# Optimization experiments

Measured on AMD Instinct MI355X. Metric: run time of the kernel, lower is better.

## Reference

```python
import jax, jax.numpy as jnp
import numpy as np

HIDDEN = 3584
NUM_HEADS = 28
NUM_KV_HEADS = 4
HEAD_DIM = 128
ROPE_THETA = 1000000.0
B, S = 2, 2048


def setup_inputs() -> dict:
    key = jax.random.key(0)
    k1, k2, k3, k4 = jax.random.split(key, 4)
    q_size = NUM_HEADS * HEAD_DIM
    kv_size = NUM_KV_HEADS * HEAD_DIM
    return {
        "positions": jnp.arange(B * S, dtype=jnp.int32).reshape(B, S),
        "hidden_states": jax.random.normal(k1, (B, S, HIDDEN), dtype=jnp.float32),
        "w_qkv": jax.random.normal(k2, (HIDDEN, q_size + 2 * kv_size), dtype=jnp.float32) * (HIDDEN ** -0.5),
        "b_qkv": jax.random.normal(k3, (q_size + 2 * kv_size,), dtype=jnp.float32) * 0.02,
        "w_o": jax.random.normal(k4, (q_size, HIDDEN), dtype=jnp.float32) * (q_size ** -0.5),
    }


def _rope_cos_sin(positions):
    # NeoX-style rotary embedding, rotary_dim == head_dim
    half = HEAD_DIM // 2
    inv_freq = 1.0 / (ROPE_THETA ** (jnp.arange(0, half, dtype=jnp.float32) * 2.0 / HEAD_DIM))
    angles = positions.astype(jnp.float32)[..., None] * inv_freq  # [B, S, half]
    return jnp.cos(angles), jnp.sin(angles)


def _apply_rope(x, cos, sin):
    # x: [B, S, H, D]; cos/sin: [B, S, half] -> broadcast over heads
    x1, x2 = jnp.split(x, 2, axis=-1)
    c = cos[:, :, None, :]
    s = sin[:, :, None, :]
    return jnp.concatenate([x1 * c - x2 * s, x2 * c + x1 * s], axis=-1)


def reference(positions, hidden_states, w_qkv, b_qkv, w_o):
    q_size = NUM_HEADS * HEAD_DIM
    kv_size = NUM_KV_HEADS * HEAD_DIM
    scaling = HEAD_DIM ** -0.5
    groups = NUM_HEADS // NUM_KV_HEADS

    qkv = hidden_states @ w_qkv + b_qkv  # [B, S, q+2kv]
    q, k, v = jnp.split(qkv, [q_size, q_size + kv_size], axis=-1)
    q = q.reshape(B, S, NUM_HEADS, HEAD_DIM)
    k = k.reshape(B, S, NUM_KV_HEADS, HEAD_DIM)
    v = v.reshape(B, S, NUM_KV_HEADS, HEAD_DIM)

    cos, sin = _rope_cos_sin(positions)
    q = _apply_rope(q, cos, sin)
    k = _apply_rope(k, cos, sin)

    # GQA: group query heads over kv heads. q: [B, S, Hkv, G, D]
    qg = q.reshape(B, S, NUM_KV_HEADS, groups, HEAD_DIM)
    scores = jnp.einsum("bqhgd,bkhd->bhgqk", qg, k) * scaling  # [B, Hkv, G, S, S]
    causal = jnp.tril(jnp.ones((S, S), dtype=bool))
    scores = jnp.where(causal, scores, jnp.finfo(scores.dtype).min)
    probs = jax.nn.softmax(scores, axis=-1)
    o = jnp.einsum("bhgqk,bkhd->bqhgd", probs, v)  # [B, S, Hkv, G, D]
    o = o.reshape(B, S, NUM_HEADS * HEAD_DIM)
    return o @ w_o  # [B, S, HIDDEN]
```

## Files before the change

kernel.cpp:

```cpp
#include <hip/hip_runtime.h>

typedef unsigned short u16;
typedef unsigned int u32;
typedef __bf16 bf16x8 __attribute__((ext_vector_type(8)));
typedef float f32x4 __attribute__((ext_vector_type(4)));

#define NHEAD 28
#define NKVH 4
#define HD 128
#define NB 2
#define NS 2048
#define NTOK 4096
#define HIDDEN_DIM 3584
#define QKVW 4608
#define QSZ 3584
#define KOFF 3584
#define VOFF 4096
#define VSLAB (NTOK * 512)
#define NJOBS 896
#define ATTN_BLOCKS 768
#define QSCALE_L2E 0.12751744f

__device__ __forceinline__ float bf2f(u16 u) {
  u32 x = ((u32)u) << 16; float f; __builtin_memcpy(&f, &x, 4); return f;
}
__device__ __forceinline__ u16 f2bf(float f) {
  u32 x; __builtin_memcpy(&x, &f, 4);
  x += 0x7FFFu + ((x >> 16) & 1u);
  return (u16)(x >> 16);
}
__device__ __forceinline__ u32 pack2bf(float a, float b) {
  __bf16 lo = (__bf16)a, hi = (__bf16)b;
  u16 ul, uh;
  __builtin_memcpy(&ul, &lo, 2); __builtin_memcpy(&uh, &hi, 2);
  return (u32)ul | ((u32)uh << 16);
}
__device__ __forceinline__ void async16(const void* g, void* lds) {
  __builtin_amdgcn_global_load_lds((const __attribute__((address_space(1))) void*)g,
                                   (__attribute__((address_space(3))) void*)lds,
                                   16, 0, 0);
}

#define SB __builtin_amdgcn_sched_barrier(0)
#define BAR do { SB; __builtin_amdgcn_s_barrier(); SB; } while (0)

__global__ void cast_f32_bf16(const float* __restrict__ in, u16* __restrict__ out) {
  int i = (blockIdx.x * 256 + threadIdx.x) * 4;
  float4 v = *(const float4*)(in + i);
  u32 p0 = (u32)f2bf(v.x) | ((u32)f2bf(v.y) << 16);
  u32 p1 = (u32)f2bf(v.z) | ((u32)f2bf(v.w) << 16);
  uint2 r; r.x = p0; r.y = p1;
  *(uint2*)(out + i) = r;
}

__global__ void transpose_cast(const float* __restrict__ in, u16* __restrict__ out,
                               int R, int C) {
  __shared__ float tile[32][33];
  int tx = threadIdx.x & 31, ty = threadIdx.x >> 5;
  int c0 = blockIdx.x * 32, r0 = blockIdx.y * 32;
#pragma unroll
  for (int i = 0; i < 32; i += 8)
    tile[ty + i][tx] = in[(size_t)(r0 + ty + i) * C + c0 + tx];
  __syncthreads();
#pragma unroll
  for (int i = 0; i < 32; i += 8)
    out[(size_t)(c0 + ty + i) * R + r0 + tx] = f2bf(tile[tx][ty + i]);
}

__global__ void rope_table(const int* __restrict__ positions,
                           float* __restrict__ cs, float* __restrict__ sn,
                           int* __restrict__ ctr) {
  if (blockIdx.x == 0 && threadIdx.x == 0) *ctr = 0;
  int idx = blockIdx.x * 256 + threadIdx.x;
  int t = idx >> 6, i = idx & 63;
  float p = (float)positions[t];
  float inv = expf(-(float)i * (13.815510557964274f / 64.f));
  float a = p * inv;
  cs[idx] = cosf(a);
  sn[idx] = sinf(a);
}

__global__ void rope_kernel(u16* __restrict__ qkv, const float* __restrict__ cs,
                            const float* __restrict__ sn) {
  int w = threadIdx.x >> 6, l = threadIdx.x & 63;
  int rid = blockIdx.x * 4 + w;
  int t = rid >> 5, hh = rid & 31;
  size_t base = (size_t)t * QKVW + (hh < NHEAD ? hh * HD : KOFF + (hh - NHEAD) * HD);
  float x1 = bf2f(qkv[base + l]), x2 = bf2f(qkv[base + l + 64]);
  float c = cs[t * 64 + l], s = sn[t * 64 + l];
  float y1 = x1 * c - x2 * s;
  float y2 = x2 * c + x1 * s;
  if (hh < NHEAD) { y1 *= QSCALE_L2E; y2 *= QSCALE_L2E; }
  qkv[base + l] = f2bf(y1);
  qkv[base + l + 64] = f2bf(y2);
}

template <int MODE>
__global__ __launch_bounds__(512, 2) void gemm256(
    const u16* __restrict__ A, const u16* __restrict__ Bt,
    const float* __restrict__ bias, u16* __restrict__ outb,
    float* __restrict__ outf, int M, int Next, int Kst, int ldc, int NT) {
  __shared__ __align__(16) u16 Al[2][256 * 64];
  __shared__ __align__(16) u16 Bl[2][256 * 64];
  const int tid = threadIdx.x;
  const int l = tid & 63, w = tid >> 6;
  const int g = l >> 4, r = l & 15;
  const int wm = w >> 2, wn = w & 3;
  const int nbx = Next >> 8;
  const int cpx = (int)gridDim.x >> 3;
  const int bid = ((int)blockIdx.x & 7) * cpx + ((int)blockIdx.x >> 3);
  int bx, by, kbase;
  float* outp = outf;
  if (MODE == 2) {
    const int tps = nbx * (M >> 8);
    const int ks = bid / tps, rem = bid % tps;
    by = rem / nbx; bx = rem % nbx;
    kbase = ks * (NT << 6);
    outp = outf + (size_t)ks * M * Next;
  } else {
    bx = bid % nbx; by = bid / nbx; kbase = 0;
  }
  const int row0 = by * 256, col0 = bx * 256;

  f32x4 acc[8][4] = {};
  bf16x8 af[4][2];
  bf16x8 bfr[2][2][2];

  auto stageU = [&](const u16* mb, int base0, char* ldsMat, int h, int t) {
#pragma unroll
    for (int q = 0; q < 2; ++q) {
      const int idx = q * 512 + tid;
      const int rho = h * 128 + (idx >> 3);
      const int sl = (idx & 7) ^ (rho & 7);
      async16(mb + (size_t)(base0 + rho) * Kst + kbase + t * 64 + sl * 8,
              ldsMat + (size_t)(t & 1) * 32768 + h * 16384 + idx * 16);
    }
  };

#define READ_A(s, rh)                                                           \
  _Pragma("unroll") for (int fr = 0; fr < 4; ++fr) {                            \
    const int row_ = (rh) * 128 + wm * 64 + fr * 16 + r;                        \
    _Pragma("unroll") for (int kk = 0; kk < 2; ++kk) {                          \
      const int sl_ = (kk * 4 + g) ^ (row_ & 7);                                \
      af[fr][kk] = *(const bf16x8*)((const char*)Al + (s) * 32768 +             \
                                    row_ * 128 + sl_ * 16);                     \
    }                                                                           \
  }
#define READ_B(s, ch)                                                           \
  _Pragma("unroll") for (int fc = 0; fc < 2; ++fc) {                            \
    const int col_ = (ch) * 128 + wn * 32 + fc * 16 + r;                        \
    _Pragma("unroll") for (int kk = 0; kk < 2; ++kk) {                          \
      const int sl_ = (kk * 4 + g) ^ (col_ & 7);                                \
      bfr[ch][fc][kk] = *(const bf16x8*)((const char*)Bl + (s) * 32768 +        \
                                         col_ * 128 + sl_ * 16);                \
    }                                                                           \
  }
#define MFMA_Q(rh, ch)                                                          \
  __builtin_amdgcn_s_setprio(1);                                                \
  _Pragma("unroll") for (int fr = 0; fr < 4; ++fr)                              \
  _Pragma("unroll") for (int fc = 0; fc < 2; ++fc)                              \
  _Pragma("unroll") for (int kk = 0; kk < 2; ++kk)                              \
    acc[(rh) * 4 + fr][(ch) * 2 + fc] = __builtin_amdgcn_mfma_f32_16x16x32_bf16( \
        af[fr][kk], bfr[ch][fc][kk], acc[(rh) * 4 + fr][(ch) * 2 + fc], 0, 0, 0);\
  __builtin_amdgcn_s_setprio(0);

  stageU(A, row0, (char*)Al, 0, 0); stageU(A, row0, (char*)Al, 1, 0);
  stageU(Bt, col0, (char*)Bl, 0, 0); stageU(Bt, col0, (char*)Bl, 1, 0);
  stageU(A, row0, (char*)Al, 0, 1); stageU(Bt, col0, (char*)Bl, 0, 1);
  SB; asm volatile("s_waitcnt vmcnt(4)" ::: "memory");
  BAR;

  for (int t = 0; t < NT; ++t) {
    const int s = t & 1;
    READ_A(s, 0); READ_B(s, 0);
    if (t + 1 < NT) stageU(A, row0, (char*)Al, 1, t + 1);
    BAR; MFMA_Q(0, 0); BAR;
    READ_B(s, 1);
    if (t + 1 < NT) stageU(Bt, col0, (char*)Bl, 1, t + 1);
    BAR; MFMA_Q(0, 1); BAR;
    READ_A(s, 1);
    if (t + 2 < NT) stageU(A, row0, (char*)Al, 0, t + 2);
    BAR; MFMA_Q(1, 0); BAR;
    if (t + 2 < NT) stageU(Bt, col0, (char*)Bl, 0, t + 2);
    BAR; MFMA_Q(1, 1);
    if (t < NT - 2)        { SB; asm volatile("s_waitcnt vmcnt(4)" ::: "memory"); }
    else if (t == NT - 2)  { SB; asm volatile("s_waitcnt vmcnt(0)" ::: "memory"); }
    BAR;
  }
  SB; asm volatile("s_waitcnt vmcnt(0)" ::: "memory");

#pragma unroll
  for (int m = 0; m < 8; ++m) {
    const int row = row0 + (m >> 2) * 128 + wm * 64 + (m & 3) * 16 + g * 4;
#pragma unroll
    for (int n = 0; n < 4; ++n) {
      const int col = col0 + (n >> 1) * 128 + wn * 32 + (n & 1) * 16 + r;
      const float bb = (MODE == 0) ? bias[col] : 0.f;
#pragma unroll
      for (int j = 0; j < 4; ++j) {
        float v = acc[m][n][j] + bb;
        if (MODE == 0) outb[(size_t)(row + j) * ldc + col] = f2bf(v);
        else           outp[(size_t)(row + j) * ldc + col] = v;
      }
    }
  }
}

__global__ void v_reduce(const float* __restrict__ slabs, const float* __restrict__ bias,
                         u16* __restrict__ vtg) {
  __shared__ float tile[32][33];
  const int tx = threadIdx.x & 31, ty = threadIdx.x >> 5;
  const int c0 = blockIdx.x * 32;
  const int r0 = blockIdx.y * 32;
#pragma unroll
  for (int i = 0; i < 32; i += 8) {
    const size_t idx = (size_t)(r0 + ty + i) * 512 + c0 + tx;
    float s = slabs[idx] + slabs[idx + VSLAB] + slabs[idx + 2 * VSLAB] +
              slabs[idx + 3 * VSLAB];
    tile[ty + i][tx] = s + bias[VOFF + c0 + tx];
  }
  __syncthreads();
#pragma unroll
  for (int i = 0; i < 32; i += 8) {
    const int col = c0 + ty + i;
    const int row = r0 + tx;
    vtg[((size_t)((((row >> 11) * NKVH) + (col >> 7)) * HD + (col & 127))) * NS +
        (row & 2047)] = f2bf(tile[tx][ty + i]);
  }
}

__global__ __launch_bounds__(512) void attn_kernel(const u16* __restrict__ qkv,
                                                   const u16* __restrict__ vtg,
                                                   u16* __restrict__ Oh,
                                                   int* __restrict__ ctr) {
  __shared__ __align__(16) u16 Ks[2][64 * 128];
  __shared__ __align__(16) u16 Vt[128 * 64];
  __shared__ int s_job;
  const int tid = threadIdx.x, l = tid & 63, w = tid >> 6;
  const int g = l >> 4, r = l & 15;
  const int srcA = r + ((l & 16) << 1);
  const int srcB = srcA + 16;
  const bool hi = (l & 32) != 0;

  for (;;) {
    if (tid == 0) s_job = atomicAdd(ctr, 1);
    __syncthreads();
    const int jid = s_job;
    if (jid >= NJOBS) return;
    const int qtr = jid / 56;
    const int qt = 15 - qtr;
    const int bh = jid - qtr * 56;
    const int h = bh % NHEAD, b = bh / NHEAD;
    const int kvh = h / 7;
    const int q0 = qt * 128;

    const int qrow = q0 + w * 16 + r;
    const size_t qbase = (size_t)(b * NS + qrow) * QKVW + h * HD;
    bf16x8 qf[4];
#pragma unroll
    for (int ks = 0; ks < 4; ++ks)
      qf[ks] = *(const bf16x8*)(qkv + qbase + ks * 32 + g * 8);

    const u16* kb0 = qkv + (size_t)(b * NS) * QKVW + KOFF + kvh * HD;
    const u16* vb0 = vtg + (size_t)((b * NKVH + kvh) * HD) * NS;

    f32x4 oacc[8] = {};
    float mrun = -1e30f, lsum = 0.f;

    const int nkv = 2 * qt + 2;

    auto stageK = [&](u16* kdst, int kv0) {
#pragma unroll
      for (int i = 0; i < 2; ++i) {
        const int li = (w * 2 + i) * 64 + l;
        const int rr = li >> 4, c = li & 15;
        async16(kb0 + (size_t)(kv0 + rr) * QKVW + ((c ^ (rr & 7)) << 3),
                (char*)kdst + (w * 2 + i) * 1024);
      }
    };
    auto stageV = [&](int kv0) {
#pragma unroll
      for (int i = 0; i < 2; ++i) {
        const int li = (w * 2 + i) * 64 + l;
        const int d = li >> 3, c = li & 7;
        async16(vb0 + (size_t)d * NS + kv0 + ((c ^ (d & 7)) << 3),
                (char*)Vt + (w * 2 + i) * 1024);
      }
    };

    stageK(Ks[0], 0);
    int cur = 0;

    for (int kvt = 0; kvt < nkv; ++kvt) {
      const int kv0 = kvt * 64;
      asm volatile("s_waitcnt vmcnt(0) lgkmcnt(0)" ::: "memory");
      __builtin_amdgcn_s_barrier();
      __builtin_amdgcn_sched_barrier(0);

      stageV(kv0);
      const bool haveNext = (kvt + 1 < nkv);
      if (haveNext) stageK(Ks[cur ^ 1], kv0 + 64);

      const bool active = kv0 <= q0 + w * 16 + 15;

      union { u32 wrd[4]; bf16x8 v; } pf[2];
      if (active) {
        f32x4 sacc[4] = {};
        const char* ksB = (const char*)Ks[cur];
        __builtin_amdgcn_s_setprio(1);
#pragma unroll
        for (int n = 0; n < 4; ++n) {
          const int key = n * 16 + r;
          const int sw = (key & 7) << 4;
#pragma unroll
          for (int ks = 0; ks < 4; ++ks) {
            bf16x8 kf = *(const bf16x8*)(ksB + key * 256 + ((ks * 64 + g * 16) ^ sw));
            sacc[n] = __builtin_amdgcn_mfma_f32_16x16x32_bf16(kf, qf[ks], sacc[n], 0, 0, 0);
          }
        }
        __builtin_amdgcn_s_setprio(0);
        if (kv0 + 63 > q0 + w * 16) {
#pragma unroll
          for (int n = 0; n < 4; ++n) {
            const int key_g = kv0 + n * 16 + g * 4;
#pragma unroll
            for (int j = 0; j < 4; ++j)
              if (key_g + j > qrow) sacc[n][j] = -1e30f;
          }
        }
        float mx = fmaxf(fmaxf(sacc[0][0], sacc[0][1]), fmaxf(sacc[0][2], sacc[0][3]));
#pragma unroll
        for (int n = 1; n < 4; ++n)
          mx = fmaxf(mx, fmaxf(fmaxf(sacc[n][0], sacc[n][1]), fmaxf(sacc[n][2], sacc[n][3])));
        if (!__all(mx <= mrun + 8.0f)) {
          mx = fmaxf(mx, __shfl_xor(mx, 16, 64));
          mx = fmaxf(mx, __shfl_xor(mx, 32, 64));
          const float mnew = fmaxf(mrun, mx);
          const float scale = __builtin_amdgcn_exp2f(mrun - mnew);
          mrun = mnew;
          lsum *= scale;
#pragma unroll
          for (int dt = 0; dt < 8; ++dt) oacc[dt] *= scale;
        }
#pragma unroll
        for (int n = 0; n < 4; ++n)
#pragma unroll
          for (int j = 0; j < 4; ++j) {
            float p = __builtin_amdgcn_exp2f(sacc[n][j] - mrun);
            sacc[n][j] = p;
            lsum += p;
          }

        u32 pk[4][2];
#pragma unroll
        for (int n = 0; n < 4; ++n) {
          pk[n][0] = pack2bf(sacc[n][0], sacc[n][1]);
          pk[n][1] = pack2bf(sacc[n][2], sacc[n][3]);
        }
#pragma unroll
        for (int ks2 = 0; ks2 < 2; ++ks2) {
          const int n0 = 2 * ks2, n1 = 2 * ks2 + 1;
#pragma unroll
          for (int hh2 = 0; hh2 < 2; ++hh2) {
            u32 a0 = (u32)__shfl((int)pk[n0][hh2], srcA, 64);
            u32 a1 = (u32)__shfl((int)pk[n1][hh2], srcA, 64);
            pf[ks2].wrd[hh2] = hi ? a1 : a0;
            u32 b0 = (u32)__shfl((int)pk[n0][hh2], srcB, 64);
            u32 b1 = (u32)__shfl((int)pk[n1][hh2], srcB, 64);
            pf[ks2].wrd[2 + hh2] = hi ? b1 : b0;
          }
        }
      }

      if (haveNext) asm volatile("s_waitcnt vmcnt(2)" ::: "memory");
      else          asm volatile("s_waitcnt vmcnt(0)" ::: "memory");
      __builtin_amdgcn_s_barrier();
      __builtin_amdgcn_sched_barrier(0);
      if (active) {
        const char* vtB = (const char*)Vt;
        __builtin_amdgcn_s_setprio(1);
#pragma unroll
        for (int ks2 = 0; ks2 < 2; ++ks2) {
#pragma unroll
          for (int dt = 0; dt < 8; ++dt) {
            const int d = dt * 16 + r;
            bf16x8 vf = *(const bf16x8*)(vtB + d * 128 +
                                         ((ks2 * 64 + g * 16) ^ ((d & 7) << 4)));
            oacc[dt] = __builtin_amdgcn_mfma_f32_16x16x32_bf16(vf, pf[ks2].v, oacc[dt], 0, 0, 0);
          }
        }
        __builtin_amdgcn_s_setprio(0);
      }
      cur ^= 1;
    }

    float lr = lsum;
    lr += __shfl_xor(lr, 16, 64);
    lr += __shfl_xor(lr, 32, 64);
    const float inv = 1.f / lr;
    const size_t obase = (size_t)(b * NS + qrow) * QSZ + h * HD;
#pragma unroll
    for (int dt = 0; dt < 8; ++dt) {
      uint2 r2;
      r2.x = pack2bf(oacc[dt][0] * inv, oacc[dt][1] * inv);
      r2.y = pack2bf(oacc[dt][2] * inv, oacc[dt][3] * inv);
      *(uint2*)(Oh + obase + dt * 16 + 4 * g) = r2;
    }
  }
}

extern "C" void kernel_launch(void* const* d_in, const int* in_sizes, int n_in,
                              void* d_out, int out_size, void* d_ws, size_t ws_size,
                              hipStream_t stream) {
  const int* positions = (const int*)d_in[0];
  const float* hidden = (const float*)d_in[1];
  const float* w_qkv = (const float*)d_in[2];
  const float* b_qkv = (const float*)d_in[3];
  const float* w_o = (const float*)d_in[4];
  float* out = (float*)d_out;

  char* ws = (char*)d_ws;
  const size_t XB_OFF = 0;
  const size_t WQT_OFF = 29360128;
  const size_t QKV_OFF = WQT_OFF + 33030144;
  const size_t CS_OFF = QKV_OFF + 37748736;
  const size_t SN_OFF = CS_OFF + 1048576;
  const size_t CTR_OFF = SN_OFF + 1048576;
  const size_t WS_NEED = CTR_OFF + 64;
  if (ws_size < WS_NEED) return;

  u16* Xb = (u16*)(ws + XB_OFF);
  u16* WoT = (u16*)(ws + XB_OFF);
  u16* WqT = (u16*)(ws + WQT_OFF);
  u16* Oh = (u16*)(ws + WQT_OFF);
  u16* qkvb = (u16*)(ws + QKV_OFF);
  float* cs = (float*)(ws + CS_OFF);
  float* sn = (float*)(ws + SN_OFF);
  int* ctr = (int*)(ws + CTR_OFF);
  u16* vtg = (u16*)d_out;
  float* vslabs = (float*)((char*)d_out + 4194304);

  cast_f32_bf16<<<14336, 256, 0, stream>>>(hidden, Xb);
  transpose_cast<<<dim3(QKVW / 32, HIDDEN_DIM / 32), 256, 0, stream>>>(w_qkv, WqT, HIDDEN_DIM, QKVW);
  rope_table<<<(NTOK * 64) / 256, 256, 0, stream>>>(positions, cs, sn, ctr);

  gemm256<0><<<256, 512, 0, stream>>>(
      Xb, WqT, b_qkv, qkvb, nullptr, NTOK, 4096, HIDDEN_DIM, QKVW, HIDDEN_DIM / 64);

  gemm256<2><<<128, 512, 0, stream>>>(
      Xb, WqT + (size_t)VOFF * HIDDEN_DIM, nullptr, nullptr, vslabs,
      NTOK, 512, HIDDEN_DIM, 512, HIDDEN_DIM / 64 / 4);

  v_reduce<<<dim3(512 / 32, NTOK / 32), 256, 0, stream>>>(vslabs, b_qkv, vtg);

  rope_kernel<<<(NTOK * 32) / 4, 256, 0, stream>>>(qkvb, cs, sn);

  transpose_cast<<<dim3(HIDDEN_DIM / 32, QSZ / 32), 256, 0, stream>>>(w_o, WoT, QSZ, HIDDEN_DIM);

  attn_kernel<<<ATTN_BLOCKS, 512, 0, stream>>>(qkvb, vtg, Oh, ctr);

  gemm256<1><<<(HIDDEN_DIM / 256) * (NTOK / 256), 512, 0, stream>>>(
      Oh, WoT, nullptr, nullptr, out, NTOK, HIDDEN_DIM, QSZ, HIDDEN_DIM, QSZ / 64);
}
```

Baseline: 446.3 us.

## Double-buffer V tiles in LDS and prefetch K/V one tile ahead

The V tile becomes an LDS double buffer, and both K and V for the next key tile are issued asynchronously before the current tile is computed. Previously V was loaded and waited on within the same iteration. The vmcnt waits are retuned for this: wait for K at the top of the loop and for V before the PV MFMAs. Per-thread global address pointers are precomputed and advanced by increments. The larger LDS footprint cuts the persistent grid from 768 to 512 blocks, trading occupancy for better overlap of loads and compute.

Result: no change. 444.6 us (-0.4%).

```diff
diff --git a/kernel.cpp b/kernel.cpp
--- a/kernel.cpp
+++ b/kernel.cpp
@@ -18,7 +18,7 @@
 #define VOFF 4096
 #define VSLAB (NTOK * 512)
 #define NJOBS 896
-#define ATTN_BLOCKS 768
+#define ATTN_BLOCKS 512
 #define QSCALE_L2E 0.12751744f
 
 __device__ __forceinline__ float bf2f(u16 u) {
@@ -234,7 +234,7 @@
                                                    u16* __restrict__ Oh,
                                                    int* __restrict__ ctr) {
   __shared__ __align__(16) u16 Ks[2][64 * 128];
-  __shared__ __align__(16) u16 Vt[128 * 64];
+  __shared__ __align__(16) u16 Vt[2][128 * 64];
   __shared__ int s_job;
   const int tid = threadIdx.x, l = tid & 63, w = tid >> 6;
   const int g = l >> 4, r = l & 15;
@@ -264,42 +264,48 @@
     const u16* kb0 = qkv + (size_t)(b * NS) * QKVW + KOFF + kvh * HD;
     const u16* vb0 = vtg + (size_t)((b * NKVH + kvh) * HD) * NS;
 
+    const u16* kap[2];
+    const u16* vap[2];
+#pragma unroll
+    for (int i = 0; i < 2; ++i) {
+      const int li = (w * 2 + i) * 64 + l;
+      const int rr = li >> 4, c = li & 15;
+      kap[i] = kb0 + (size_t)rr * QKVW + ((c ^ (rr & 7)) << 3);
+      const int d = li >> 3, c2 = li & 7;
+      vap[i] = vb0 + (size_t)d * NS + ((c2 ^ (d & 7)) << 3);
+    }
+
     f32x4 oacc[8] = {};
     float mrun = -1e30f, lsum = 0.f;
 
     const int nkv = 2 * qt + 2;
 
-    auto stageK = [&](u16* kdst, int kv0) {
+    auto stageK = [&](u16* kdst) {
 #pragma unroll
       for (int i = 0; i < 2; ++i) {
-        const int li = (w * 2 + i) * 64 + l;
-        const int rr = li >> 4, c = li & 15;
-        async16(kb0 + (size_t)(kv0 + rr) * QKVW + ((c ^ (rr & 7)) << 3),
-                (char*)kdst + (w * 2 + i) * 1024);
+        async16(kap[i], (char*)kdst + (w * 2 + i) * 1024);
+        kap[i] += 64 * QKVW;
       }
     };
-    auto stageV = [&](int kv0) {
+    auto stageV = [&](u16* vdst) {
 #pragma unroll
       for (int i = 0; i < 2; ++i) {
-        const int li = (w * 2 + i) * 64 + l;
-        const int d = li >> 3, c = li & 7;
-        async16(vb0 + (size_t)d * NS + kv0 + ((c ^ (d & 7)) << 3),
-                (char*)Vt + (w * 2 + i) * 1024);
+        async16(vap[i], (char*)vdst + (w * 2 + i) * 1024);
+        vap[i] += 64;
       }
     };
 
-    stageK(Ks[0], 0);
+    stageK(Ks[0]); stageV(Vt[0]);
     int cur = 0;
 
     for (int kvt = 0; kvt < nkv; ++kvt) {
       const int kv0 = kvt * 64;
-      asm volatile("s_waitcnt vmcnt(0) lgkmcnt(0)" ::: "memory");
+      asm volatile("s_waitcnt vmcnt(2)" ::: "memory");
       __builtin_amdgcn_s_barrier();
       __builtin_amdgcn_sched_barrier(0);
 
-      stageV(kv0);
       const bool haveNext = (kvt + 1 < nkv);
-      if (haveNext) stageK(Ks[cur ^ 1], kv0 + 64);
+      if (haveNext) { stageK(Ks[cur ^ 1]); stageV(Vt[cur ^ 1]); }
 
       const bool active = kv0 <= q0 + w * 16 + 15;
 
@@ -372,12 +378,12 @@
         }
       }
 
-      if (haveNext) asm volatile("s_waitcnt vmcnt(2)" ::: "memory");
+      if (haveNext) asm volatile("s_waitcnt vmcnt(4)" ::: "memory");
       else          asm volatile("s_waitcnt vmcnt(0)" ::: "memory");
       __builtin_amdgcn_s_barrier();
       __builtin_amdgcn_sched_barrier(0);
       if (active) {
-        const char* vtB = (const char*)Vt;
+        const char* vtB = (const char*)Vt[cur];
         __builtin_amdgcn_s_setprio(1);
 #pragma unroll
         for (int ks2 = 0; ks2 < 2; ++ks2) {
```
